# Kernel optimization log

Measured on AMD Instinct MI355X. Metric: run time of the kernel, lower is better.

The kernel has to match this reference:

```python
import jax, jax.numpy as jnp
import numpy as np

N_QUBITS = 4
B = 524288


def ry_mat(theta):
    # theta: scalar or (B,) -> (..., 2, 2) complex64
    c = jnp.cos(theta / 2).astype(jnp.complex64)
    s = jnp.sin(theta / 2).astype(jnp.complex64)
    return jnp.stack([jnp.stack([c, -s], -1), jnp.stack([s, c], -1)], -2)


def rz_mat(theta):
    e = jnp.exp(-0.5j * theta.astype(jnp.complex64))
    z = jnp.zeros_like(e)
    return jnp.stack([jnp.stack([e, z], -1), jnp.stack([z, jnp.conj(e)], -1)], -2)


def apply_shared(state, gate, wire):
    # state: (B, 2,2,2,2); gate: (2,2) shared across batch
    state = jnp.moveaxis(state, 1 + wire, -1)
    state = jnp.einsum('...a,ca->...c', state, gate)
    return jnp.moveaxis(state, -1, 1 + wire)


def apply_batched(state, gate, wire):
    # gate: (B, 2, 2), per-sample angles
    state = jnp.moveaxis(state, 1 + wire, -1)
    state = jnp.einsum('b...a,bca->b...c', state, gate)
    return jnp.moveaxis(state, -1, 1 + wire)


def cnot_01(state):
    # control wire 0 (axis 1), target wire 1 (axis 2): flip target when control=1
    return jnp.concatenate([state[:, :1], jnp.flip(state[:, 1:], axis=2)], axis=1)


def circuit(x, weights):
    # batched 4-qubit state-vector simulation; state shape (B, 2,2,2,2)
    b = x.shape[0]
    state = jnp.zeros((b,) + (2,) * N_QUBITS, jnp.complex64).at[:, 0, 0, 0, 0].set(1.0)
    # data-encoding RY layer (per-sample angles)
    for i in range(N_QUBITS):
        state = apply_batched(state, ry_mat(x[:, i]), i)
    # two repeats of (RZ, RY per wire) + CNOT(0,1); only weights[0,:,0:2] is used (faithful to source)
    for _rep in range(2):
        for i in range(N_QUBITS):
            state = apply_shared(state, rz_mat(weights[0, i, 0]), i)
            state = apply_shared(state, ry_mat(weights[0, i, 1]), i)
        state = cnot_01(state)
    probs = jnp.real(state * jnp.conj(state))  # (B,2,2,2,2)
    zexp = []
    for i in range(N_QUBITS):
        axes = tuple(a for a in range(1, 1 + N_QUBITS) if a != 1 + i)
        marg = probs.sum(axis=axes)  # (B, 2)
        zexp.append(marg[:, 0] - marg[:, 1])
    return jnp.stack(zexp, axis=-1).astype(jnp.float32)  # (B, 4)


def setup_inputs() -> dict:
    key = jax.random.key(0)
    k1, k2, k3, k4 = jax.random.split(key, 4)
    return {
        'x': jax.random.normal(k1, (B, N_QUBITS), dtype=jnp.float32),
        'weights': jax.random.normal(k2, (2, N_QUBITS, 4), dtype=jnp.float32),
        'head_w': jax.random.normal(k3, (2, N_QUBITS), dtype=jnp.float32) * 0.5,
        'head_b': jax.random.normal(k4, (2,), dtype=jnp.float32) * 0.1,
    }


def reference(x, weights, head_w, head_b):
    q = circuit(x, weights)            # (B, 4) PauliZ expectations
    return q @ head_w.T + head_b       # Linear(4, 2)
```

## Files before the change

### kernel.cpp

```cpp
#include <hip/hip_runtime.h>

#define NQ  4
#define DIM 16

__global__ __launch_bounds__(256) void prep_kernel(
    const float* __restrict__ weights,
    const float* __restrict__ head_w,
    const float* __restrict__ head_b,
    float* __restrict__ T)
{
    __shared__ float Ure[DIM][DIM];
    __shared__ float Uim[DIM][DIM];
    __shared__ float sw[2][DIM];
    __shared__ float sA[2][DIM][DIM];

    const int tid = threadIdx.x;

    if (tid < DIM) {
        const int j = tid;
        float szv[NQ], czv[NQ], syv[NQ], cyv[NQ];
        #pragma unroll
        for (int i = 0; i < NQ; ++i) {
            __sincosf(0.5f * weights[i * 4 + 0], &szv[i], &czv[i]);
            __sincosf(0.5f * weights[i * 4 + 1], &syv[i], &cyv[i]);
        }
        float sre[DIM], sim[DIM];
        #pragma unroll
        for (int m = 0; m < DIM; ++m) { sre[m] = (m == j) ? 1.f : 0.f; sim[m] = 0.f; }
        #pragma unroll
        for (int rep = 0; rep < 2; ++rep) {
            #pragma unroll
            for (int i = 0; i < NQ; ++i) {
                const float sz = szv[i], cz = czv[i];
                const float sy = syv[i], cy = cyv[i];
                const int bit = 8 >> i;
                #pragma unroll
                for (int m = 0; m < DIM; ++m) {
                    if (m & bit) continue;
                    const int m1 = m | bit;
                    const float are = sre[m],  aim = sim[m];
                    const float bre = sre[m1], bim = sim[m1];
                    const float n0re = are * cz + aim * sz;
                    const float n0im = aim * cz - are * sz;
                    const float n1re = bre * cz - bim * sz;
                    const float n1im = bim * cz + bre * sz;
                    sre[m]  = cy * n0re - sy * n1re;
                    sim[m]  = cy * n0im - sy * n1im;
                    sre[m1] = sy * n0re + cy * n1re;
                    sim[m1] = sy * n0im + cy * n1im;
                }
            }
            #pragma unroll
            for (int m = 0; m < DIM; ++m) {
                if ((m & 8) && !(m & 4)) {
                    const int m2 = m | 4;
                    const float tr = sre[m], ti = sim[m];
                    sre[m] = sre[m2]; sim[m] = sim[m2];
                    sre[m2] = tr;     sim[m2] = ti;
                }
            }
        }
        #pragma unroll
        for (int m = 0; m < DIM; ++m) { Ure[m][j] = sre[m]; Uim[m][j] = sim[m]; }
    } else if (tid < DIM + 32) {
        const int t = tid - DIM;
        const int o = t >> 4, m = t & 15;
        float w = 0.f;
        #pragma unroll
        for (int i = 0; i < NQ; ++i) {
            const float hw = head_w[o * 4 + i];
            w += ((m >> (3 - i)) & 1) ? -hw : hw;
        }
        sw[o][m] = w;
    }
    __syncthreads();

    #pragma unroll
    for (int it = 0; it < 2; ++it) {
        const int idx = it * 256 + tid;
        const int o  = idx >> 8;
        const int jj = (idx >> 4) & 15;
        const int kk = idx & 15;
        float acc = 0.f;
        #pragma unroll
        for (int m = 0; m < DIM; ++m)
            acc = fmaf(sw[o][m],
                       Ure[m][jj] * Ure[m][kk] + Uim[m][jj] * Uim[m][kk], acc);
        sA[o][jj][kk] = acc;
    }
    __syncthreads();

    if (tid < 2 * 81) {
        const int o  = tid / 81;
        const int r  = tid % 81;
        const int a0 = r / 27, a1 = (r / 9) % 3, a2 = (r / 3) % 3, a3 = r % 3;
        const int xm = ((a0 == 2) << 3) | ((a1 == 2) << 2) | ((a2 == 2) << 1) | (a3 == 2);
        const int sm = ((a0 == 1) << 3) | ((a1 == 1) << 2) | ((a2 == 1) << 1) | (a3 == 1);
        float acc = 0.f;
        #pragma unroll
        for (int jj = 0; jj < DIM; ++jj) {
            const float s = (__popc(jj & sm) & 1) ? -1.f : 1.f;
            acc += s * sA[o][jj][jj ^ xm];
        }
        float t = acc * 0.0625f;
        if (r == 0) t += head_b[o];
        T[tid] = t;
    }
}

__device__ __forceinline__ float2 qeval(const float4 xv, const float* __restrict__ T)
{
    float c0, s0, c1, s1, c2, s2, c3, s3;
    __sincosf(xv.x, &s0, &c0);
    __sincosf(xv.y, &s1, &c1);
    __sincosf(xv.z, &s2, &c2);
    __sincosf(xv.w, &s3, &c3);

    float r[2];
    #pragma unroll
    for (int o = 0; o < 2; ++o) {
        float w2[9];
        #pragma unroll
        for (int t = 0; t < 9; ++t) {
            float a = fmaf(s3, T[o * 81 + 9 * t + 2], fmaf(c3, T[o * 81 + 9 * t + 1], T[o * 81 + 9 * t + 0]));
            w2[t] = a;
        }
        float w3[27];
        #pragma unroll
        for (int t = 0; t < 27; ++t)
            w3[t] = fmaf(s3, T[o * 81 + 3 * t + 2],
                    fmaf(c3, T[o * 81 + 3 * t + 1], T[o * 81 + 3 * t + 0]));
        #pragma unroll
        for (int t = 0; t < 9; ++t)
            w2[t] = fmaf(s2, w3[3 * t + 2], fmaf(c2, w3[3 * t + 1], w3[3 * t + 0]));
        float w1[3];
        #pragma unroll
        for (int t = 0; t < 3; ++t)
            w1[t] = fmaf(s1, w2[3 * t + 2], fmaf(c1, w2[3 * t + 1], w2[3 * t + 0]));
        r[o] = fmaf(s0, w1[2], fmaf(c0, w1[1], w1[0]));
    }
    return make_float2(r[0], r[1]);
}

__global__ __launch_bounds__(256) void qmain2_kernel(
    const float4* __restrict__ x4,
    const float* __restrict__ T,
    float4* __restrict__ out4)
{
    const int t = blockIdx.x * 256 + threadIdx.x;
    const float4 xa = x4[2 * t];
    const float4 xb = x4[2 * t + 1];
    const float2 ra = qeval(xa, T);
    const float2 rb = qeval(xb, T);
    out4[t] = make_float4(ra.x, ra.y, rb.x, rb.y);
}

__global__ __launch_bounds__(256) void qmain1_kernel(
    const float4* __restrict__ x4,
    const float* __restrict__ T,
    float2* __restrict__ out,
    const int Btot)
{
    const int b = blockIdx.x * 256 + threadIdx.x;
    if (b >= Btot) return;
    out[b] = qeval(x4[b], T);
}

extern "C" void kernel_launch(void* const* d_in, const int* in_sizes, int n_in,
                              void* d_out, int out_size, void* d_ws, size_t ws_size,
                              hipStream_t stream) {
    const float* x       = (const float*)d_in[0];
    const float* weights = (const float*)d_in[1];
    const float* head_w  = (const float*)d_in[2];
    const float* head_b  = (const float*)d_in[3];
    float* out = (float*)d_out;
    float* T   = (float*)d_ws;

    const int Btot = in_sizes[0] / 4;

    prep_kernel<<<1, 256, 0, stream>>>(weights, head_w, head_b, T);

    if ((Btot & 511) == 0) {
        qmain2_kernel<<<Btot / 512, 256, 0, stream>>>(
            (const float4*)x, T, (float4*)out);
    } else {
        qmain1_kernel<<<(Btot + 255) / 256, 256, 0, stream>>>(
            (const float4*)x, T, (float2*)out, Btot);
    }
}
```

Baseline: 70.35 us.

## Fuse coefficient prep into main kernel with redundant per-block prep and register-cached table

Removes the separate single-block prep kernel. Every block now recomputes the 16x16 unitary with wavefront shuffles (one amplitude per lane), builds the 162-entry coefficient table in shared memory, and copies it into registers. Each thread then processes 4 samples in a grid-stride loop. This removes a kernel launch and the dependent global round trip of T, at the cost of redundant prep work in each of 512 blocks and heavy register pressure from the 164-float register array.

```diff
diff --git a/kernel.cpp b/kernel.cpp
--- a/kernel.cpp
+++ b/kernel.cpp
@@ -3,75 +3,96 @@
 #define NQ  4
 #define DIM 16
 
-__global__ __launch_bounds__(256) void prep_kernel(
-    const float* __restrict__ weights,
-    const float* __restrict__ head_w,
-    const float* __restrict__ head_b,
-    float* __restrict__ T)
+
+__device__ __forceinline__ float2 qeval_reg(const float4 xv, const float* Tr)
+{
+    float c0, s0, c1, s1, c2, s2, c3, s3;
+    __sincosf(xv.x, &s0, &c0);
+    __sincosf(xv.y, &s1, &c1);
+    __sincosf(xv.z, &s2, &c2);
+    __sincosf(xv.w, &s3, &c3);
+
+    float r[2];
+    #pragma unroll
+    for (int o = 0; o < 2; ++o) {
+        float w3[27];
+        #pragma unroll
+        for (int t = 0; t < 27; ++t)
+            w3[t] = fmaf(s3, Tr[o * 81 + 3 * t + 2],
+                    fmaf(c3, Tr[o * 81 + 3 * t + 1], Tr[o * 81 + 3 * t + 0]));
+        float w2[9];
+        #pragma unroll
+        for (int t = 0; t < 9; ++t)
+            w2[t] = fmaf(s2, w3[3 * t + 2], fmaf(c2, w3[3 * t + 1], w3[3 * t + 0]));
+        float w1[3];
+        #pragma unroll
+        for (int t = 0; t < 3; ++t)
+            w1[t] = fmaf(s1, w2[3 * t + 2], fmaf(c1, w2[3 * t + 1], w2[3 * t + 0]));
+        r[o] = fmaf(s0, w1[2], fmaf(c0, w1[1], w1[0]));
+    }
+    return make_float2(r[0], r[1]);
+}
+
+__global__ __launch_bounds__(256, 2) void fused_kernel(
+    const float4* __restrict__ x4,
+    const float*  __restrict__ weights,
+    const float*  __restrict__ head_w,
+    const float*  __restrict__ head_b,
+    float2*       __restrict__ out2,
+    const int Btot)
 {
     __shared__ float Ure[DIM][DIM];
     __shared__ float Uim[DIM][DIM];
-    __shared__ float sw[2][DIM];
+    __shared__ float sw2[2][DIM];
     __shared__ float sA[2][DIM][DIM];
+    __shared__ __align__(16) float sT[164];
 
     const int tid = threadIdx.x;
+    const int j = tid >> 4;
+    const int m = tid & 15;
 
-    if (tid < DIM) {
-        const int j = tid;
+    {
         float szv[NQ], czv[NQ], syv[NQ], cyv[NQ];
         #pragma unroll
         for (int i = 0; i < NQ; ++i) {
             __sincosf(0.5f * weights[i * 4 + 0], &szv[i], &czv[i]);
             __sincosf(0.5f * weights[i * 4 + 1], &syv[i], &cyv[i]);
         }
-        float sre[DIM], sim[DIM];
-        #pragma unroll
-        for (int m = 0; m < DIM; ++m) { sre[m] = (m == j) ? 1.f : 0.f; sim[m] = 0.f; }
+        float sre = (m == j) ? 1.f : 0.f;
+        float sim = 0.f;
         #pragma unroll
         for (int rep = 0; rep < 2; ++rep) {
             #pragma unroll
             for (int i = 0; i < NQ; ++i) {
-                const float sz = szv[i], cz = czv[i];
-                const float sy = syv[i], cy = cyv[i];
                 const int bit = 8 >> i;
-                #pragma unroll
-                for (int m = 0; m < DIM; ++m) {
-                    if (m & bit) continue;
-                    const int m1 = m | bit;
-                    const float are = sre[m],  aim = sim[m];
-                    const float bre = sre[m1], bim = sim[m1];
-                    const float n0re = are * cz + aim * sz;
-                    const float n0im = aim * cz - are * sz;
-                    const float n1re = bre * cz - bim * sz;
-                    const float n1im = bim * cz + bre * sz;
-                    sre[m]  = cy * n0re - sy * n1re;
-                    sim[m]  = cy * n0im - sy * n1im;
-                    sre[m1] = sy * n0re + cy * n1re;
-                    sim[m1] = sy * n0im + cy * n1im;
-                }
+                const bool hi = (m & bit) != 0;
+                const float cz = czv[i], sz = szv[i];
+                const float cy = cyv[i], sy = syv[i];
+                const float e = hi ? -sz : sz;
+                const float zre = fmaf( e, sim, sre * cz);
+                const float zim = fmaf(-e, sre, sim * cz);
+                const float pzre = __shfl_xor(zre, bit);
+                const float pzim = __shfl_xor(zim, bit);
+                const float f = hi ? sy : -sy;
+                sre = fmaf(f, pzre, cy * zre);
+                sim = fmaf(f, pzim, cy * zim);
             }
-            #pragma unroll
-            for (int m = 0; m < DIM; ++m) {
-                if ((m & 8) && !(m & 4)) {
-                    const int m2 = m | 4;
-                    const float tr = sre[m], ti = sim[m];
-                    sre[m] = sre[m2]; sim[m] = sim[m2];
-                    sre[m2] = tr;     sim[m2] = ti;
-                }
-            }
+            const float pre = __shfl_xor(sre, 4);
+            const float pim = __shfl_xor(sim, 4);
+            if (m & 8) { sre = pre; sim = pim; }
         }
-        #pragma unroll
-        for (int m = 0; m < DIM; ++m) { Ure[m][j] = sre[m]; Uim[m][j] = sim[m]; }
-    } else if (tid < DIM + 32) {
-        const int t = tid - DIM;
-        const int o = t >> 4, m = t & 15;
+        Ure[m][j] = sre;
+        Uim[m][j] = sim;
+    }
+    if (tid < 32) {
+        const int o = tid >> 4, mm = tid & 15;
         float w = 0.f;
         #pragma unroll
         for (int i = 0; i < NQ; ++i) {
             const float hw = head_w[o * 4 + i];
-            w += ((m >> (3 - i)) & 1) ? -hw : hw;
+            w += ((mm >> (3 - i)) & 1) ? -hw : hw;
         }
-        sw[o][m] = w;
+        sw2[o][mm] = w;
     }
     __syncthreads();
 
@@ -83,9 +104,9 @@
         const int kk = idx & 15;
         float acc = 0.f;
         #pragma unroll
-        for (int m = 0; m < DIM; ++m)
-            acc = fmaf(sw[o][m],
-                       Ure[m][jj] * Ure[m][kk] + Uim[m][jj] * Uim[m][kk], acc);
+        for (int mm = 0; mm < DIM; ++mm)
+            acc = fmaf(sw2[o][mm],
+                       Ure[mm][jj] * Ure[mm][kk] + Uim[mm][jj] * Uim[mm][kk], acc);
         sA[o][jj][kk] = acc;
     }
     __syncthreads();
@@ -99,71 +120,39 @@
         float acc = 0.f;
         #pragma unroll
         for (int jj = 0; jj < DIM; ++jj) {
-            const float s = (__popc(jj & sm) & 1) ? -1.f : 1.f;
-            acc += s * sA[o][jj][jj ^ xm];
+            const float sgn = (__popc(jj & sm) & 1) ? -1.f : 1.f;
+            acc += sgn * sA[o][jj][jj ^ xm];
         }
         float t = acc * 0.0625f;
         if (r == 0) t += head_b[o];
-        T[tid] = t;
+        sT[tid] = t;
     }
-}
+    if (tid >= 162 && tid < 164) sT[tid] = 0.f;
+    __syncthreads();
 
-__device__ __forceinline__ float2 qeval(const float4 xv, const float* __restrict__ T)
-{
-    float c0, s0, c1, s1, c2, s2, c3, s3;
-    __sincosf(xv.x, &s0, &c0);
-    __sincosf(xv.y, &s1, &c1);
-    __sincosf(xv.z, &s2, &c2);
-    __sincosf(xv.w, &s3, &c3);
+    float Tr[164];
+    {
+        const float4* sT4 = reinterpret_cast<const float4*>(sT);
+        #pragma unroll
+        for (int q = 0; q < 41; ++q) {
+            const float4 v = sT4[q];
+            Tr[4 * q + 0] = v.x;
+            Tr[4 * q + 1] = v.y;
+            Tr[4 * q + 2] = v.z;
+            Tr[4 * q + 3] = v.w;
+        }
+    }
 
-    float r[2];
-    #pragma unroll
-    for (int o = 0; o < 2; ++o) {
-        float w2[9];
-        #pragma unroll
-        for (int t = 0; t < 9; ++t) {
-            float a = fmaf(s3, T[o * 81 + 9 * t + 2], fmaf(c3, T[o * 81 + 9 * t + 1], T[o * 81 + 9 * t + 0]));
-            w2[t] = a;
+    const int GT   = gridDim.x << 8;
+    const int base = (blockIdx.x << 8) + tid;
+    #pragma unroll 1
+    for (int k = 0; k < 4; ++k) {
+        const int s = base + k * GT;
+        if (s < Btot) {
+            const float4 xv = x4[s];
+            out2[s] = qeval_reg(xv, Tr);
         }
-        float w3[27];
-        #pragma unroll
-        for (int t = 0; t < 27; ++t)
-            w3[t] = fmaf(s3, T[o * 81 + 3 * t + 2],
-                    fmaf(c3, T[o * 81 + 3 * t + 1], T[o * 81 + 3 * t + 0]));
-        #pragma unroll
-        for (int t = 0; t < 9; ++t)
-            w2[t] = fmaf(s2, w3[3 * t + 2], fmaf(c2, w3[3 * t + 1], w3[3 * t + 0]));
-        float w1[3];
-        #pragma unroll
-        for (int t = 0; t < 3; ++t)
-            w1[t] = fmaf(s1, w2[3 * t + 2], fmaf(c1, w2[3 * t + 1], w2[3 * t + 0]));
-        r[o] = fmaf(s0, w1[2], fmaf(c0, w1[1], w1[0]));
     }
-    return make_float2(r[0], r[1]);
-}
-
-__global__ __launch_bounds__(256) void qmain2_kernel(
-    const float4* __restrict__ x4,
-    const float* __restrict__ T,
-    float4* __restrict__ out4)
-{
-    const int t = blockIdx.x * 256 + threadIdx.x;
-    const float4 xa = x4[2 * t];
-    const float4 xb = x4[2 * t + 1];
-    const float2 ra = qeval(xa, T);
-    const float2 rb = qeval(xb, T);
-    out4[t] = make_float4(ra.x, ra.y, rb.x, rb.y);
-}
-
-__global__ __launch_bounds__(256) void qmain1_kernel(
-    const float4* __restrict__ x4,
-    const float* __restrict__ T,
-    float2* __restrict__ out,
-    const int Btot)
-{
-    const int b = blockIdx.x * 256 + threadIdx.x;
-    if (b >= Btot) return;
-    out[b] = qeval(x4[b], T);
 }
 
 extern "C" void kernel_launch(void* const* d_in, const int* in_sizes, int n_in,
@@ -174,17 +163,11 @@
     const float* head_w  = (const float*)d_in[2];
     const float* head_b  = (const float*)d_in[3];
     float* out = (float*)d_out;
-    float* T   = (float*)d_ws;
+    (void)d_ws; (void)ws_size;
 
-    const int Btot = in_sizes[0] / 4;
+    const int Btot   = in_sizes[0] / 4;
+    const int blocks = (Btot + 1023) / 1024;
 
-    prep_kernel<<<1, 256, 0, stream>>>(weights, head_w, head_b, T);
-
-    if ((Btot & 511) == 0) {
-        qmain2_kernel<<<Btot / 512, 256, 0, stream>>>(
-            (const float4*)x, T, (float4*)out);
-    } else {
-        qmain1_kernel<<<(Btot + 255) / 256, 256, 0, stream>>>(
-            (const float4*)x, T, (float2*)out, Btot);
-    }
+    fused_kernel<<<blocks, 256, 0, stream>>>(
+        (const float4*)x, weights, head_w, head_b, (float2*)out, Btot);
 }
```

New measurement: 68.05 us. -3.3%, faster.
